# Optimization experiments

Hardware: AMD Instinct MI355X
Metric: run time of the kernel (lower is better)

## Reference

```python
import jax, jax.numpy as jnp
import numpy as np

B = 8192          # batch
CIN = 256         # in_channels
COUT = 64         # out_channels
K = 3             # kernel_size
NK = 4            # num_kernels
HIDDEN = int(CIN * 0.25)   # attention hidden = int(in_channels*ratio) = 64
TEMP = 34.0       # attention temperature
KAN_IN = 64 * 4   # base*4 = flattened conv output (COUT*2*2)
GRID_SIZE, SPLINE_ORDER = 5, 3
GMIN, GMAX = -1.0, 1.0
NUM_BASES = GRID_SIZE + SPLINE_ORDER  # 8


def setup_inputs() -> dict:
    key = jax.random.key(0)
    ks = jax.random.split(key, 8)
    s = 0.05
    return {
        "x": jax.random.normal(ks[0], (B, CIN, 4, 4), jnp.float32),
        # dynamic-conv kernel bank [num_kernels, out, in, k, k]
        "weight": jax.random.normal(ks[1], (NK, COUT, CIN, K, K), jnp.float32) * s,
        "bias": jnp.zeros((NK, COUT), jnp.float32),
        # Attention2D: GAP -> fc1 (1x1 conv == linear) -> ReLU -> fc2 -> softmax(/T)
        "fc1_w": jax.random.normal(ks[2], (HIDDEN, CIN), jnp.float32) * s,
        "fc1_b": jnp.zeros((HIDDEN,), jnp.float32),
        "fc2_w": jax.random.normal(ks[3], (NK, HIDDEN), jnp.float32) * s,
        "fc2_b": jnp.zeros((NK,), jnp.float32),
        # KANLinear params (efficient-KAN style)
        "kan_base_w": jax.random.normal(ks[4], (COUT, KAN_IN), jnp.float32) * s,
        "kan_spline_w": jax.random.normal(ks[5], (COUT, KAN_IN, NUM_BASES), jnp.float32) * s,
        "kan_spline_scaler": jnp.ones((COUT, KAN_IN), jnp.float32),
    }


def _bspline_bases(x):
    """Cox-de Boor B-spline bases; x [B, F] -> [B, F, GRID_SIZE+SPLINE_ORDER]."""
    h = (GMAX - GMIN) / GRID_SIZE
    # extended grid, shared across features: length grid_size + 2*order + 1 = 12
    grid = jnp.arange(-SPLINE_ORDER, GRID_SIZE + SPLINE_ORDER + 1, dtype=x.dtype) * h + GMIN
    xe = x[..., None]  # [B, F, 1]
    bases = ((xe >= grid[:-1]) & (xe < grid[1:])).astype(x.dtype)  # order 0
    for k in range(1, SPLINE_ORDER + 1):
        left = (xe - grid[: -(k + 1)]) / (grid[k:-1] - grid[: -(k + 1)]) * bases[..., :-1]
        right = (grid[k + 1:] - xe) / (grid[k + 1:] - grid[1:-k]) * bases[..., 1:]
        bases = left + right
    return bases  # [B, F, 8]


def reference(x, weight, bias, fc1_w, fc1_b, fc2_w, fc2_b,
              kan_base_w, kan_spline_w, kan_spline_scaler):
    b = x.shape[0]
    # --- Attention2D: softmax over kernel bank ---
    pooled = x.mean(axis=(2, 3))                                  # [B, CIN]
    hid = jax.nn.relu(pooled @ fc1_w.T + fc1_b)                   # [B, HIDDEN]
    attn = jax.nn.softmax((hid @ fc2_w.T + fc2_b) / TEMP, axis=-1)  # [B, NK]
    # --- per-sample dynamic conv, fused form ---
    # sum_k a[b,k] * conv(x, W_k) == conv with per-sample aggregated weight
    w_all = weight.reshape(NK * COUT, CIN, K, K)
    y = jax.lax.conv_general_dilated(
        x, w_all, window_strides=(1, 1), padding="VALID",
        dimension_numbers=("NCHW", "OIHW", "NCHW"))                # [B, NK*COUT, 2, 2]
    y = y.reshape(b, NK, COUT, y.shape[-2], y.shape[-1])
    conv_out = jnp.einsum("bk,bkohw->bohw", attn, y)
    conv_out = conv_out + (attn @ bias)[:, :, None, None]          # aggregated bias
    # --- KANLinear on flattened conv output ---
    feat = conv_out.reshape(b, -1)                                 # [B, 256]
    base_out = jax.nn.silu(feat) @ kan_base_w.T                    # [B, COUT]
    bases = _bspline_bases(feat)                                   # [B, 256, 8]
    spline_out = jnp.einsum("big,oig->bo", bases,
                            kan_spline_w * kan_spline_scaler[..., None])
    return base_out + spline_out                                   # [B, COUT]
```

## Files before the change

### kernel.cpp

```cpp
#include <hip/hip_runtime.h>

#define BT   8192
#define MS   16
#define XBUF (MS * 656)

typedef _Float16 half8  __attribute__((ext_vector_type(8)));
typedef _Float16 half4v __attribute__((ext_vector_type(4)));
typedef float    floatx4  __attribute__((ext_vector_type(4)));
typedef float    floatx16 __attribute__((ext_vector_type(16)));

__global__ __launch_bounds__(256) void prep_kernel(
    const float* __restrict__ weight, const float* __restrict__ base_w,
    const float* __restrict__ spline_w, const float* __restrict__ scaler,
    const float* __restrict__ fc1_w,
    _Float16* __restrict__ W3, _Float16* __restrict__ Wk3,
    _Float16* __restrict__ Wf3)
{
    const int bb = blockIdx.x;
    const int tid = threadIdx.x;
    if (bb < 256) {
        const int n = bb;
        const int c = tid;
        const float* src = weight + ((size_t)n * 256 + c) * 9;
        const int cc = c >> 5, ci = c & 31;
        #pragma unroll
        for (int ij = 0; ij < 9; ++ij) {
            W3[((size_t)(cc * 9 + ij) * 256 + n) * 32 + ci] = (_Float16)src[ij];
        }
    } else if (bb < 328) {
        const int st = bb - 256;
        #pragma unroll
        for (int u = 0; u < 8; ++u) {
            const int idx = u * 256 + tid;
            const int n = idx >> 5, kk = idx & 31;
            const int k = st * 32 + kk;
            float v;
            if (k < 256) {
                v = base_w[n * 256 + k];
            } else {
                const int r = k - 256;
                const int i = r >> 3, g = r & 7;
                v = spline_w[((size_t)n * 256 + i) * 8 + g] * scaler[n * 256 + i];
            }
            Wk3[(size_t)st * 2048 + idx] = (_Float16)v;
        }
    } else {
        const int st2 = bb - 328;
        #pragma unroll
        for (int u = 0; u < 8; ++u) {
            const int idx = u * 256 + tid;
            const int n = idx >> 5, kk = idx & 31;
            Wf3[(size_t)st2 * 2048 + idx] = (_Float16)fc1_w[n * 256 + st2 * 32 + kk];
        }
    }
}

__device__ __forceinline__ void bases8c(float xv, _Float16* dst) {
    const float t = (xv + 2.2f) * 2.5f;
    const float ft = floorf(t);
    const int idx = (int)ft;
    const float u = t - ft, v = 1.f - u;
    const float u2 = u * u, v2 = v * v;
    const float c3 = u2 * u * (1.f / 6.f);
    const float c2 = (1.f / 6.f) + 0.5f * (u + u2 - u2 * u);
    const float c1 = (1.f / 6.f) + 0.5f * (v + v2 - v2 * v);
    const float c0 = v2 * v * (1.f / 6.f);
    half8 hb;
    #pragma unroll
    for (int tt = 0; tt < 8; ++tt) {
        const int d = idx - tt;
        float b = 0.f;
        b = (d == 0) ? c3 : b;
        b = (d == 1) ? c2 : b;
        b = (d == 2) ? c1 : b;
        b = (d == 3) ? c0 : b;
        hb[tt] = (_Float16)b;
    }
    *(half8*)dst = hb;
}

__global__ __launch_bounds__(512, 4) void fused_kernel(
    const float* __restrict__ x, const _Float16* __restrict__ W3,
    const _Float16* __restrict__ Wk3, const _Float16* __restrict__ Wf3,
    const float* __restrict__ bias, const float* __restrict__ fc1_b,
    const float* __restrict__ fc2_w, const float* __restrict__ fc2_b,
    float* __restrict__ out)
{
    __shared__ __align__(16) char smem[MS * 2312 * 2];
    __shared__ float hid_lds[MS * 68];
    __shared__ float attn_s[MS][4];

    _Float16* Xs  = (_Float16*)smem;
    _Float16* Pl  = (_Float16*)(smem + 2 * XBUF * 2);
    _Float16* Act = (_Float16*)smem;

    const int tid = threadIdx.x;
    const int wv = tid >> 6, lane = tid & 63;
    const int nl = lane & 15, q = lane >> 4;
    const int cg = wv & 3, kh = wv >> 2;
    const int b0 = blockIdx.x * MS;

    const int posr = nl & 3;
    const int aLane = (nl >> 2) * 656 + ((posr >> 1) * 4 + (posr & 1)) * 40 + q * 8;
    const int lbW = (cg * 16 + nl) * 32 + q * 8;

    const int s_ = tid >> 5, cch = tid & 31;
    const float* xg = x + ((size_t)(b0 + s_) * 256 + cch) * 16;

    floatx4 acc[4][4];
    #pragma unroll
    for (int rt = 0; rt < 4; ++rt)
        #pragma unroll
        for (int kb = 0; kb < 4; ++kb)
            acc[rt][kb] = floatx4{0.f, 0.f, 0.f, 0.f};

    half8 bcur[4];
    {
        const _Float16* w0 = W3 + (size_t)(kh ? 5 : 0) * 8192 + lbW;
        #pragma unroll
        for (int kb = 0; kb < 4; ++kb)
            bcur[kb] = *(const half8*)(w0 + kb * 2048);
    }

    floatx16 r = *(const floatx16*)xg;
    {
        _Float16* xd = &Xs[s_ * 656 + cch];
        #pragma unroll
        for (int p = 0; p < 16; ++p) xd[p * 40] = (_Float16)r[p];
        float sm = 0.f;
        #pragma unroll
        for (int p = 0; p < 16; ++p) sm += r[p];
        Pl[s_ * 264 + cch] = (_Float16)(sm * (1.0f / 16.0f));
    }
    r = *(const floatx16*)(xg + 512);
    __syncthreads();

    #pragma unroll 1
    for (int cc = 0; cc < 8; ++cc) {
        const int cur = cc & 1;
        if (cc < 7) {
            _Float16* xd = &Xs[(cur ^ 1) * XBUF + s_ * 656 + cch];
            #pragma unroll
            for (int p = 0; p < 16; ++p) xd[p * 40] = (_Float16)r[p];
            float sm = 0.f;
            #pragma unroll
            for (int p = 0; p < 16; ++p) sm += r[p];
            Pl[s_ * 264 + (cc + 1) * 32 + cch] = (_Float16)(sm * (1.0f / 16.0f));
        }
        if (cc < 6) r = *(const floatx16*)(xg + (cc + 2) * 512);

        const _Float16* wst = W3 + (size_t)cc * 9 * 8192 + lbW;
        const _Float16* xb = &Xs[cur * XBUF + aLane];

        #pragma unroll
        for (int i = 0; i < 4; ++i) {
            const int ijn = (i < 3) ? (kh ? 6 + i : 1 + i) : 4;
            half8 bnxt[4];
            #pragma unroll
            for (int kb = 0; kb < 4; ++kb)
                bnxt[kb] = *(const half8*)(wst + (size_t)ijn * 8192 + kb * 2048);

            const int p0 = kh ? ((int[4]){6, 8, 9, 10})[i]
                              : ((int[4]){0, 1, 2, 4})[i];

            {
                const half8 aF0 = *(const half8*)&xb[0 * 2624 + p0 * 40];
                const half8 aF1 = *(const half8*)&xb[1 * 2624 + p0 * 40];
                #pragma unroll
                for (int kb = 0; kb < 4; ++kb)
                    acc[0][kb] = __builtin_amdgcn_mfma_f32_16x16x32_f16(aF0, bcur[kb], acc[0][kb], 0, 0, 0);
                #pragma unroll
                for (int kb = 0; kb < 4; ++kb)
                    acc[1][kb] = __builtin_amdgcn_mfma_f32_16x16x32_f16(aF1, bcur[kb], acc[1][kb], 0, 0, 0);
            }
            {
                const half8 aF2 = *(const half8*)&xb[2 * 2624 + p0 * 40];
                const half8 aF3 = *(const half8*)&xb[3 * 2624 + p0 * 40];
                #pragma unroll
                for (int kb = 0; kb < 4; ++kb)
                    acc[2][kb] = __builtin_amdgcn_mfma_f32_16x16x32_f16(aF2, bcur[kb], acc[2][kb], 0, 0, 0);
                #pragma unroll
                for (int kb = 0; kb < 4; ++kb)
                    acc[3][kb] = __builtin_amdgcn_mfma_f32_16x16x32_f16(aF3, bcur[kb], acc[3][kb], 0, 0, 0);
            }
            #pragma unroll
            for (int kb = 0; kb < 4; ++kb) bcur[kb] = bnxt[kb];
        }

        {
            const _Float16* wnx = (cc < 7)
                ? (W3 + (size_t)(cc + 1) * 9 * 8192 + (size_t)(kh ? 5 : 0) * 8192 + lbW)
                : (W3 + lbW);
            half8 bnxt[4];
            #pragma unroll
            for (int kb = 0; kb < 4; ++kb)
                bnxt[kb] = *(const half8*)(wnx + kb * 2048);

            if (kh == 0) {
                const half8 aF0 = *(const half8*)&xb[0 * 2624 + 5 * 40];
                const half8 aF1 = *(const half8*)&xb[1 * 2624 + 5 * 40];
                #pragma unroll
                for (int kb = 0; kb < 4; ++kb)
                    acc[0][kb] = __builtin_amdgcn_mfma_f32_16x16x32_f16(aF0, bcur[kb], acc[0][kb], 0, 0, 0);
                #pragma unroll
                for (int kb = 0; kb < 4; ++kb)
                    acc[1][kb] = __builtin_amdgcn_mfma_f32_16x16x32_f16(aF1, bcur[kb], acc[1][kb], 0, 0, 0);
            } else {
                const half8 aF2 = *(const half8*)&xb[2 * 2624 + 5 * 40];
                const half8 aF3 = *(const half8*)&xb[3 * 2624 + 5 * 40];
                #pragma unroll
                for (int kb = 0; kb < 4; ++kb)
                    acc[2][kb] = __builtin_amdgcn_mfma_f32_16x16x32_f16(aF2, bcur[kb], acc[2][kb], 0, 0, 0);
                #pragma unroll
                for (int kb = 0; kb < 4; ++kb)
                    acc[3][kb] = __builtin_amdgcn_mfma_f32_16x16x32_f16(aF3, bcur[kb], acc[3][kb], 0, 0, 0);
            }
            #pragma unroll
            for (int kb = 0; kb < 4; ++kb) bcur[kb] = bnxt[kb];
        }
        __syncthreads();
    }

    if (kh == 0) {
        floatx4 a1 = floatx4{0.f, 0.f, 0.f, 0.f};
        const _Float16* wfb = Wf3 + ((cg * 16 + nl) * 32 + q * 8);
        const _Float16* pb = &Pl[nl * 264 + q * 8];
        #pragma unroll
        for (int st = 0; st < 8; ++st) {
            const half8 aF = *(const half8*)(pb + st * 32);
            const half8 bF = *(const half8*)(wfb + st * 2048);
            a1 = __builtin_amdgcn_mfma_f32_16x16x32_f16(aF, bF, a1, 0, 0, 0);
        }
        const int h = cg * 16 + nl;
        const float fb = fc1_b[h];
        #pragma unroll
        for (int reg = 0; reg < 4; ++reg)
            hid_lds[(q * 4 + reg) * 68 + h] = fmaxf(a1[reg] + fb, 0.f);
    }
    __syncthreads();

    if (wv == 0) {
        const int s = lane >> 2, kb = lane & 3;
        float l = fc2_b[kb];
        #pragma unroll 8
        for (int h = 0; h < 64; ++h) l += hid_lds[s * 68 + h] * fc2_w[kb * 64 + h];
        float m = fmaxf(l, __shfl_xor(l, 1));
        m = fmaxf(m, __shfl_xor(m, 2));
        const float e = __expf((l - m) * (1.0f / 34.0f));
        float sm = e + __shfl_xor(e, 1);
        sm += __shfl_xor(sm, 2);
        attn_s[s][kb] = e / sm;
    }
    __syncthreads();

    const int o = cg * 16 + nl;
    if (kh == 1) {
        #pragma unroll
        for (int rt = 0; rt < 4; ++rt) {
            const int s = rt * 4 + q;
            const float a0 = attn_s[s][0], a1 = attn_s[s][1],
                        a2 = attn_s[s][2], a3 = attn_s[s][3];
            #pragma unroll
            for (int e = 0; e < 4; ++e) {
                float* slot = (float*)&Act[s * 2312 + 256 + (o * 4 + e) * 8];
                slot[0] = a0 * acc[rt][0][e] + a1 * acc[rt][1][e]
                        + a2 * acc[rt][2][e] + a3 * acc[rt][3][e];
            }
        }
    }
    __syncthreads();

    if (kh == 0) {
        const float bb0 = bias[o], bb1 = bias[64 + o], bb2 = bias[128 + o], bb3 = bias[192 + o];
        #pragma unroll
        for (int rt = 0; rt < 4; ++rt) {
            const int s = rt * 4 + q;
            const float a0 = attn_s[s][0], a1 = attn_s[s][1],
                        a2 = attn_s[s][2], a3 = attn_s[s][3];
            const float badd = a0 * bb0 + a1 * bb1 + a2 * bb2 + a3 * bb3;
            float f[4];
            #pragma unroll
            for (int e = 0; e < 4; ++e) {
                const float part = ((float*)&Act[s * 2312 + 256 + (o * 4 + e) * 8])[0];
                f[e] = a0 * acc[rt][0][e] + a1 * acc[rt][1][e]
                     + a2 * acc[rt][2][e] + a3 * acc[rt][3][e] + part + badd;
            }
            half4v sv;
            #pragma unroll
            for (int e = 0; e < 4; ++e) {
                const float ex = __expf(-f[e]);
                sv[e] = (_Float16)(f[e] * __builtin_amdgcn_rcpf(1.f + ex));
            }
            *(half4v*)&Act[s * 2312 + o * 4] = sv;
            #pragma unroll
            for (int e = 0; e < 4; ++e)
                bases8c(f[e], &Act[s * 2312 + 256 + (o * 4 + e) * 8]);
        }
    }
    __syncthreads();

    {
        floatx4 a2 = floatx4{0.f, 0.f, 0.f, 0.f};
        const _Float16* wkb = Wk3 + ((size_t)(cg * 16 + nl) * 32 + q * 8);
        const _Float16* ab = &Act[nl * 2312 + q * 8];
        const int st0 = kh * 36;
        half8 kb0 = *(const half8*)(wkb + (size_t)st0 * 2048);
        half8 kb1 = *(const half8*)(wkb + (size_t)(st0 + 1) * 2048);
        #pragma unroll 4
        for (int i = 0; i < 36; ++i) {
            half8 kb2;
            if (i < 34) kb2 = *(const half8*)(wkb + (size_t)(st0 + i + 2) * 2048);
            const half8 aF = *(const half8*)(ab + (st0 + i) * 32);
            a2 = __builtin_amdgcn_mfma_f32_16x16x32_f16(aF, kb0, a2, 0, 0, 0);
            kb0 = kb1; kb1 = kb2;
        }
        if (kh == 1) *(floatx4*)&hid_lds[cg * 256 + lane * 4] = a2;
        __syncthreads();
        if (kh == 0) {
            const floatx4 p = *(const floatx4*)&hid_lds[cg * 256 + lane * 4];
            a2 = a2 + p;
            #pragma unroll
            for (int reg = 0; reg < 4; ++reg)
                out[(size_t)(b0 + q * 4 + reg) * 64 + cg * 16 + nl] = a2[reg];
        }
    }
}

extern "C" void kernel_launch(void* const* d_in, const int* in_sizes, int n_in,
                              void* d_out, int out_size, void* d_ws, size_t ws_size,
                              hipStream_t stream) {
    const float* x          = (const float*)d_in[0];
    const float* weight     = (const float*)d_in[1];
    const float* bias       = (const float*)d_in[2];
    const float* fc1_w      = (const float*)d_in[3];
    const float* fc1_b      = (const float*)d_in[4];
    const float* fc2_w      = (const float*)d_in[5];
    const float* fc2_b      = (const float*)d_in[6];
    const float* kan_base_w = (const float*)d_in[7];
    const float* kan_spline = (const float*)d_in[8];
    const float* kan_scaler = (const float*)d_in[9];
    float* out = (float*)d_out;

    _Float16* W3  = (_Float16*)d_ws;
    _Float16* Wk3 = W3 + (size_t)72 * 8192;
    _Float16* Wf3 = Wk3 + (size_t)72 * 2048;

    prep_kernel<<<336, 256, 0, stream>>>(weight, kan_base_w, kan_spline,
                                         kan_scaler, fc1_w, W3, Wk3, Wf3);
    fused_kernel<<<BT / MS, 512, 0, stream>>>(x, W3, Wk3, Wf3, bias, fc1_b,
                                              fc2_w, fc2_b, out);
}
```

Baseline: 284.2 us.

## Split conv work across wave halves by sample rows instead of kernel taps

The two wave groups (kh) now each own half of the sample row-tiles and loop over all nine kernel taps, instead of each covering all four row-tiles over a split of the taps. This halves the accumulator registers per wave and removes the cross-wave partial-sum exchange through LDS plus one barrier. Both groups now run the silu/B-spline epilogue in parallel. In exchange, each wave loads all nine weight fragments per channel chunk, so global weight-load traffic per wave roughly doubles.

```diff
diff --git a/kernel.cpp b/kernel.cpp
--- a/kernel.cpp
+++ b/kernel.cpp
@@ -101,26 +101,24 @@
     const int b0 = blockIdx.x * MS;
 
     const int posr = nl & 3;
-    const int aLane = (nl >> 2) * 656 + ((posr >> 1) * 4 + (posr & 1)) * 40 + q * 8;
+    const int aLane = (nl >> 2) * 656 + ((posr >> 1) * 4 + (posr & 1)) * 40 + q * 8
+                    + kh * 5248;
     const int lbW = (cg * 16 + nl) * 32 + q * 8;
 
     const int s_ = tid >> 5, cch = tid & 31;
     const float* xg = x + ((size_t)(b0 + s_) * 256 + cch) * 16;
 
-    floatx4 acc[4][4];
+    floatx4 acc[2][4];
     #pragma unroll
-    for (int rt = 0; rt < 4; ++rt)
+    for (int r2 = 0; r2 < 2; ++r2)
         #pragma unroll
         for (int kb = 0; kb < 4; ++kb)
-            acc[rt][kb] = floatx4{0.f, 0.f, 0.f, 0.f};
+            acc[r2][kb] = floatx4{0.f, 0.f, 0.f, 0.f};
 
     half8 bcur[4];
-    {
-        const _Float16* w0 = W3 + (size_t)(kh ? 5 : 0) * 8192 + lbW;
-        #pragma unroll
-        for (int kb = 0; kb < 4; ++kb)
-            bcur[kb] = *(const half8*)(w0 + kb * 2048);
-    }
+    #pragma unroll
+    for (int kb = 0; kb < 4; ++kb)
+        bcur[kb] = *(const half8*)(W3 + kb * 2048 + lbW);
 
     floatx16 r = *(const floatx16*)xg;
     {
@@ -152,69 +150,27 @@
         const _Float16* wst = W3 + (size_t)cc * 9 * 8192 + lbW;
         const _Float16* xb = &Xs[cur * XBUF + aLane];
 
-        #pragma unroll
-        for (int i = 0; i < 4; ++i) {
-            const int ijn = (i < 3) ? (kh ? 6 + i : 1 + i) : 4;
-            half8 bnxt[4];
-            #pragma unroll
-            for (int kb = 0; kb < 4; ++kb)
-                bnxt[kb] = *(const half8*)(wst + (size_t)ijn * 8192 + kb * 2048);
-
-            const int p0 = kh ? ((int[4]){6, 8, 9, 10})[i]
-                              : ((int[4]){0, 1, 2, 4})[i];
-
-            {
-                const half8 aF0 = *(const half8*)&xb[0 * 2624 + p0 * 40];
-                const half8 aF1 = *(const half8*)&xb[1 * 2624 + p0 * 40];
-                #pragma unroll
-                for (int kb = 0; kb < 4; ++kb)
-                    acc[0][kb] = __builtin_amdgcn_mfma_f32_16x16x32_f16(aF0, bcur[kb], acc[0][kb], 0, 0, 0);
-                #pragma unroll
-                for (int kb = 0; kb < 4; ++kb)
-                    acc[1][kb] = __builtin_amdgcn_mfma_f32_16x16x32_f16(aF1, bcur[kb], acc[1][kb], 0, 0, 0);
-            }
-            {
-                const half8 aF2 = *(const half8*)&xb[2 * 2624 + p0 * 40];
-                const half8 aF3 = *(const half8*)&xb[3 * 2624 + p0 * 40];
-                #pragma unroll
-                for (int kb = 0; kb < 4; ++kb)
-                    acc[2][kb] = __builtin_amdgcn_mfma_f32_16x16x32_f16(aF2, bcur[kb], acc[2][kb], 0, 0, 0);
-                #pragma unroll
-                for (int kb = 0; kb < 4; ++kb)
-                    acc[3][kb] = __builtin_amdgcn_mfma_f32_16x16x32_f16(aF3, bcur[kb], acc[3][kb], 0, 0, 0);
-            }
-            #pragma unroll
-            for (int kb = 0; kb < 4; ++kb) bcur[kb] = bnxt[kb];
-        }
-
-        {
-            const _Float16* wnx = (cc < 7)
-                ? (W3 + (size_t)(cc + 1) * 9 * 8192 + (size_t)(kh ? 5 : 0) * 8192 + lbW)
-                : (W3 + lbW);
+        const int p0tab[9] = {0, 1, 2, 4, 5, 6, 8, 9, 10};
+
+        #pragma unroll
+        for (int ij = 0; ij < 9; ++ij) {
+            const _Float16* wnx = (ij == 8 && cc == 7)
+                                ? (W3 + lbW)
+                                : (wst + (size_t)(ij + 1) * 8192);
             half8 bnxt[4];
             #pragma unroll
             for (int kb = 0; kb < 4; ++kb)
                 bnxt[kb] = *(const half8*)(wnx + kb * 2048);
 
-            if (kh == 0) {
-                const half8 aF0 = *(const half8*)&xb[0 * 2624 + 5 * 40];
-                const half8 aF1 = *(const half8*)&xb[1 * 2624 + 5 * 40];
-                #pragma unroll
-                for (int kb = 0; kb < 4; ++kb)
-                    acc[0][kb] = __builtin_amdgcn_mfma_f32_16x16x32_f16(aF0, bcur[kb], acc[0][kb], 0, 0, 0);
-                #pragma unroll
-                for (int kb = 0; kb < 4; ++kb)
-                    acc[1][kb] = __builtin_amdgcn_mfma_f32_16x16x32_f16(aF1, bcur[kb], acc[1][kb], 0, 0, 0);
-            } else {
-                const half8 aF2 = *(const half8*)&xb[2 * 2624 + 5 * 40];
-                const half8 aF3 = *(const half8*)&xb[3 * 2624 + 5 * 40];
-                #pragma unroll
-                for (int kb = 0; kb < 4; ++kb)
-                    acc[2][kb] = __builtin_amdgcn_mfma_f32_16x16x32_f16(aF2, bcur[kb], acc[2][kb], 0, 0, 0);
-                #pragma unroll
-                for (int kb = 0; kb < 4; ++kb)
-                    acc[3][kb] = __builtin_amdgcn_mfma_f32_16x16x32_f16(aF3, bcur[kb], acc[3][kb], 0, 0, 0);
-            }
+            const int p0 = p0tab[ij];
+            const half8 aF0 = *(const half8*)&xb[p0 * 40];
+            const half8 aF1 = *(const half8*)&xb[2624 + p0 * 40];
+            #pragma unroll
+            for (int kb = 0; kb < 4; ++kb)
+                acc[0][kb] = __builtin_amdgcn_mfma_f32_16x16x32_f16(aF0, bcur[kb], acc[0][kb], 0, 0, 0);
+            #pragma unroll
+            for (int kb = 0; kb < 4; ++kb)
+                acc[1][kb] = __builtin_amdgcn_mfma_f32_16x16x32_f16(aF1, bcur[kb], acc[1][kb], 0, 0, 0);
             #pragma unroll
             for (int kb = 0; kb < 4; ++kb) bcur[kb] = bnxt[kb];
         }
@@ -254,36 +210,19 @@
     __syncthreads();
 
     const int o = cg * 16 + nl;
-    if (kh == 1) {
-        #pragma unroll
-        for (int rt = 0; rt < 4; ++rt) {
-            const int s = rt * 4 + q;
-            const float a0 = attn_s[s][0], a1 = attn_s[s][1],
-                        a2 = attn_s[s][2], a3 = attn_s[s][3];
-            #pragma unroll
-            for (int e = 0; e < 4; ++e) {
-                float* slot = (float*)&Act[s * 2312 + 256 + (o * 4 + e) * 8];
-                slot[0] = a0 * acc[rt][0][e] + a1 * acc[rt][1][e]
-                        + a2 * acc[rt][2][e] + a3 * acc[rt][3][e];
-            }
-        }
-    }
-    __syncthreads();
-
-    if (kh == 0) {
+    {
         const float bb0 = bias[o], bb1 = bias[64 + o], bb2 = bias[128 + o], bb3 = bias[192 + o];
         #pragma unroll
-        for (int rt = 0; rt < 4; ++rt) {
-            const int s = rt * 4 + q;
+        for (int r2 = 0; r2 < 2; ++r2) {
+            const int s = (kh * 2 + r2) * 4 + q;
             const float a0 = attn_s[s][0], a1 = attn_s[s][1],
                         a2 = attn_s[s][2], a3 = attn_s[s][3];
             const float badd = a0 * bb0 + a1 * bb1 + a2 * bb2 + a3 * bb3;
             float f[4];
             #pragma unroll
             for (int e = 0; e < 4; ++e) {
-                const float part = ((float*)&Act[s * 2312 + 256 + (o * 4 + e) * 8])[0];
-                f[e] = a0 * acc[rt][0][e] + a1 * acc[rt][1][e]
-                     + a2 * acc[rt][2][e] + a3 * acc[rt][3][e] + part + badd;
+                f[e] = a0 * acc[r2][0][e] + a1 * acc[r2][1][e]
+                     + a2 * acc[r2][2][e] + a3 * acc[r2][3][e] + badd;
             }
             half4v sv;
             #pragma unroll
```

New measurement: 274.7 us. 1.03x faster.
